# Optimization experiments

Hardware: AMD Instinct MI355X
Metric: run time of the kernel (lower is better)

The kernel has to match this reference:

```python
import jax, jax.numpy as jnp
import numpy as np

B, T, D, NPER, E = 32, 256, 1024, 64, 65536
N = B * NPER  # total nodes
LN_EPS = 1e-5


def setup_inputs() -> dict:
    key = jax.random.key(0)
    ks = jax.random.split(key, 12)
    sc = 0.02  # init scale for weights
    inp = {
        "x": jax.random.normal(ks[0], (B, T, D), jnp.float32),
        "batch": jnp.repeat(jnp.arange(B, dtype=jnp.int32), NPER),
        "edge_index": jax.random.randint(ks[1], (2, E), 0, N, dtype=jnp.int32),
        "edge_distance_vec": jax.random.normal(ks[2], (E, 3), jnp.float32),
        "edge_distance": jax.random.uniform(ks[3], (E,), jnp.float32) + 0.5,
        "natoms": NPER,
        # energy head params: LayerNorm -> Linear(D,D) -> GELU -> Linear(D,1)
        "ln_g": jnp.ones((D,), jnp.float32),
        "ln_b": jnp.zeros((D,), jnp.float32),
        "We1": jax.random.normal(ks[4], (D, D), jnp.float32) * sc,
        "be1": jnp.zeros((D,), jnp.float32),
        "We2": jax.random.normal(ks[5], (D, 1), jnp.float32) * sc,
        "be2": jnp.zeros((1,), jnp.float32),
        # forces head params: Linear(2D,D) -> GELU -> Linear(D,1)
        "Wf1": jax.random.normal(ks[6], (2 * D, D), jnp.float32) * sc,
        "bf1": jnp.zeros((D,), jnp.float32),
        "Wf2": jax.random.normal(ks[7], (D, 1), jnp.float32) * sc,
        "bf2": jnp.zeros((1,), jnp.float32),
    }
    return inp


def reference(x, batch, edge_index, edge_distance_vec, edge_distance, natoms,
              ln_g, ln_b, We1, be1, We2, be2, Wf1, bf1, Wf2, bf2):
    # ---- energy head on CLS token ----
    cls = x[:, 0]  # [B, D]
    mu = jnp.mean(cls, axis=-1, keepdims=True)
    var = jnp.mean(jnp.square(cls - mu), axis=-1, keepdims=True)
    h = (cls - mu) / jnp.sqrt(var + LN_EPS) * ln_g + ln_b
    h = jax.nn.gelu(h @ We1 + be1, approximate=False)
    energy = h @ We2 + be2  # [B, 1]

    # ---- forces head: gather node pairs -> MLP -> scale -> scatter-sum ----
    # padded_node_mask selects tokens 1..natoms per graph; boolean indexing
    # flattens row-major, identical to this slice+reshape.
    nodes = x[:, 1:1 + natoms].reshape(-1, x.shape[-1])  # [N, D]
    ei0, ei1 = edge_index[0], edge_index[1]
    edge_inputs = jnp.concatenate([nodes[ei0], nodes[ei1]], axis=1)  # [E, 2D]
    fm = jax.nn.gelu(edge_inputs @ Wf1 + bf1, approximate=False) @ Wf2 + bf2  # [E, 1]
    force_pairs = fm * edge_distance_vec / edge_distance[:, None]  # [E, 3]
    forces = jax.ops.segment_sum(force_pairs, ei0, num_segments=batch.shape[0])  # [N, 3]
    return energy, forces
```

## Files before the change

### kernel.cpp

```cpp
#include <hip/hip_runtime.h>
#include <hip/hip_fp16.h>
#include <math.h>

#define BB 32
#define TT 256
#define DD 1024
#define NNODES 2048
#define EE 65536
#define LN_EPS 1e-5f

typedef _Float16 halfx8 __attribute__((ext_vector_type(8)));
typedef __attribute__((ext_vector_type(4))) float floatx4;

__device__ __forceinline__ float gelu_fast(float x) {
    float x2 = x * x;
    float z = x * fmaf(0.10294456f, x2, 2.30211786f);
    float e = __builtin_amdgcn_exp2f(z);
    float r = __builtin_amdgcn_rcpf(1.0f + e);
    return fmaf(-x, r, x);
}

__device__ __forceinline__ __half2 gelu_h2(__half2 x) {
    const __half2 k = __float2half2_rn(-2.4554669f);
    const __half2 one = __float2half2_rn(1.0f);
    __half2 e = h2exp2(__hmul2(x, k));
    return __hmul2(x, h2rcp(__hadd2(e, one)));
}

__device__ __forceinline__ float dot2f(__half2 a, __half2 b, float c) {
#if __has_builtin(__builtin_amdgcn_fdot2)
    typedef _Float16 v2h __attribute__((ext_vector_type(2)));
    return __builtin_amdgcn_fdot2(*(v2h*)&a, *(v2h*)&b, c, false);
#else
    float2 af = __half22float2(a), bf = __half22float2(b);
    return fmaf(af.x, bf.x, fmaf(af.y, bf.y, c));
#endif
}

__device__ __forceinline__ unsigned short f32_to_h16(float f) {
    return __half_as_ushort(__float2half_rn(f));
}

__device__ __forceinline__ void load_lds16(const void* g, void* l) {
    __builtin_amdgcn_global_load_lds(
        (const __attribute__((address_space(1))) void*)g,
        (__attribute__((address_space(3))) void*)l, 16, 0, 0);
}

__global__ __launch_bounds__(256) void k1_zero_ln_prep_kernel(
    const float* __restrict__ x, const float* __restrict__ g,
    const float* __restrict__ bta, const float* __restrict__ Wf1,
    float* __restrict__ hnorm, float* __restrict__ out,
    unsigned short* __restrict__ nodesH, unsigned short* __restrict__ Wf1T) {
    __shared__ float smem[32 * 33];
    int t = threadIdx.x;
    int b = blockIdx.x;
    if (b < BB) {
        int zi = b * 256 + t;
        if (zi < BB + NNODES * 3) out[zi] = 0.0f;
        float* red = smem;
        const float* row = x + (size_t)b * TT * DD;
        float v[4];
        float s = 0.0f;
        #pragma unroll
        for (int j = 0; j < 4; ++j) { v[j] = row[t + j * 256]; s += v[j]; }
        red[t] = s; __syncthreads();
        for (int off = 128; off > 0; off >>= 1) {
            if (t < off) red[t] += red[t + off];
            __syncthreads();
        }
        float mu = red[0] * (1.0f / DD);
        __syncthreads();
        float sq = 0.0f;
        #pragma unroll
        for (int j = 0; j < 4; ++j) { float d = v[j] - mu; sq += d * d; }
        red[t] = sq; __syncthreads();
        for (int off = 128; off > 0; off >>= 1) {
            if (t < off) red[t] += red[t + off];
            __syncthreads();
        }
        float rstd = rsqrtf(red[0] * (1.0f / DD) + LN_EPS);
        #pragma unroll
        for (int j = 0; j < 4; ++j) {
            int d = t + j * 256;
            hnorm[b * DD + d] = (v[j] - mu) * rstd * g[d] + bta[d];
        }
        return;
    }
    int pb = b - BB;
    if (pb < 2048) {
        int idx4 = (pb * 256 + t) * 4;
        int i = idx4 >> 10;
        int k = idx4 & 1023;
        const float* src = x + ((size_t)(i >> 6) * TT + 1 + (i & 63)) * DD + k;
        float4 v = *(const float4*)src;
        ushort4 o;
        o.x = f32_to_h16(v.x); o.y = f32_to_h16(v.y);
        o.z = f32_to_h16(v.z); o.w = f32_to_h16(v.w);
        *(ushort4*)&nodesH[idx4] = o;
    } else {
        int q = pb - 2048;
        float (*tile)[33] = (float(*)[33])smem;
        int tx = t & 31;
        int ty = t >> 5;
        int n0 = (q & 31) * 32;
        int kg0 = (q >> 5) * 32;
        #pragma unroll
        for (int j = 0; j < 4; ++j) {
            int r = ty * 4 + j;
            tile[r][tx] = Wf1[(size_t)(kg0 + r) * DD + n0 + tx];
        }
        __syncthreads();
        int half = kg0 >> 10;
        int kk0 = kg0 & 1023;
        unsigned short* o = Wf1T + (size_t)half * DD * DD;
        #pragma unroll
        for (int j = 0; j < 4; ++j) {
            int rn = ty * 4 + j;
            o[(size_t)(n0 + rn) * DD + kk0 + tx] = f32_to_h16(tile[tx][rn]);
        }
    }
}

__global__ __launch_bounds__(512) void k2_gemm_kernel(
    const unsigned short* __restrict__ nodesH,
    const unsigned short* __restrict__ Wf1T, const float* __restrict__ bf1,
    unsigned short* __restrict__ P, const float* __restrict__ hnorm,
    const float* __restrict__ We1, float* __restrict__ He) {
    __shared__ unsigned short smem[2 * 128 * 64];
    int t = threadIdx.x;
    int b = blockIdx.x;
    if (b < 256) {
        unsigned short* As = smem;
        unsigned short* Bs = smem + 128 * 64;
        int w = t >> 6;
        int lane = t & 63;
        int quad = lane >> 4;
        int l16 = lane & 15;
        int wn = (w & 3) * 32;
        int wi = (w >> 2) * 64;
        int n0 = (b & 7) * 128;
        int i0 = ((b >> 3) & 15) * 128;
        int half = b >> 7;

        const unsigned short* Ag = Wf1T + (size_t)half * DD * DD;
        const unsigned short* Bg = nodesH;

        int sr = lane >> 3;
        int sc = (lane & 7) ^ sr;
        size_t aoff[2], boff[2];
        #pragma unroll
        for (int j = 0; j < 2; ++j) {
            int row = w * 16 + j * 8;
            aoff[j] = (size_t)(n0 + row + sr) * DD + sc * 8;
            boff[j] = (size_t)(i0 + row + sr) * DD + sc * 8;
        }

        floatx4 acc[2][4];
        #pragma unroll
        for (int a = 0; a < 2; ++a)
            #pragma unroll
            for (int c = 0; c < 4; ++c) {
                acc[a][c][0] = 0.f; acc[a][c][1] = 0.f;
                acc[a][c][2] = 0.f; acc[a][c][3] = 0.f;
            }

        for (int k0 = 0; k0 < DD; k0 += 64) {
            #pragma unroll
            for (int j = 0; j < 2; ++j) {
                int row = w * 16 + j * 8;
                load_lds16(Ag + aoff[j] + k0, (void*)(As + row * 64));
                load_lds16(Bg + boff[j] + k0, (void*)(Bs + row * 64));
            }
            __syncthreads();
            #pragma unroll
            for (int s = 0; s < 2; ++s) {
                halfx8 af[2], bfr[4];
                #pragma unroll
                for (int f = 0; f < 2; ++f) {
                    int rn = wn + f * 16 + l16;
                    af[f] = *(const halfx8*)&As[rn * 64 + ((((s << 2) | quad) ^ (rn & 7)) << 3)];
                }
                #pragma unroll
                for (int f = 0; f < 4; ++f) {
                    int ri = wi + f * 16 + l16;
                    bfr[f] = *(const halfx8*)&Bs[ri * 64 + ((((s << 2) | quad) ^ (ri & 7)) << 3)];
                }
                #pragma unroll
                for (int fa = 0; fa < 2; ++fa)
                    #pragma unroll
                    for (int fb = 0; fb < 4; ++fb)
                        acc[fa][fb] = __builtin_amdgcn_mfma_f32_16x16x32_f16(
                            af[fa], bfr[fb], acc[fa][fb], 0, 0, 0);
            }
            __syncthreads();
        }

        unsigned short* Pout = P + (size_t)half * NNODES * DD;
        #pragma unroll
        for (int fa = 0; fa < 2; ++fa) {
            int n = n0 + wn + fa * 16 + quad * 4;
            float4 badd = make_float4(0.f, 0.f, 0.f, 0.f);
            if (half == 0) badd = *(const float4*)(bf1 + n);
            #pragma unroll
            for (int fb = 0; fb < 4; ++fb) {
                int i = i0 + wi + fb * 16 + l16;
                floatx4 v = acc[fa][fb];
                ushort4 o;
                o.x = f32_to_h16(v[0] + badd.x);
                o.y = f32_to_h16(v[1] + badd.y);
                o.z = f32_to_h16(v[2] + badd.z);
                o.w = f32_to_h16(v[3] + badd.w);
                *(ushort4*)&Pout[(size_t)i * DD + n] = o;
            }
        }
        return;
    }
    {
        int q = b - 256;
        float* hs = (float*)smem;
        int col = (q & 1) * 512 + t;
        int k0 = ((q >> 1) & 15) * 64;
        int r0 = (q >> 5) * 16;
        for (int idx = t; idx < 64 * 16; idx += 512) {
            int r = idx & 15, k = idx >> 4;
            hs[idx] = hnorm[(size_t)(r0 + r) * DD + k0 + k];
        }
        __syncthreads();
        float acc[16];
        #pragma unroll
        for (int r = 0; r < 16; ++r) acc[r] = 0.0f;
        #pragma unroll 4
        for (int k = 0; k < 64; ++k) {
            float wv = We1[(size_t)(k0 + k) * DD + col];
            const float* hrow = hs + k * 16;
            #pragma unroll
            for (int j = 0; j < 4; ++j) {
                float4 h4 = *(const float4*)(hrow + j * 4);
                acc[j * 4 + 0] = fmaf(h4.x, wv, acc[j * 4 + 0]);
                acc[j * 4 + 1] = fmaf(h4.y, wv, acc[j * 4 + 1]);
                acc[j * 4 + 2] = fmaf(h4.z, wv, acc[j * 4 + 2]);
                acc[j * 4 + 3] = fmaf(h4.w, wv, acc[j * 4 + 3]);
            }
        }
        float* o = He + (size_t)((q >> 1) & 15) * 32 * DD;
        #pragma unroll
        for (int r = 0; r < 16; ++r) o[(size_t)(r0 + r) * DD + col] = acc[r];
    }
}

__global__ __launch_bounds__(256) void k3_edge_energy2_kernel(
    const unsigned short* __restrict__ P, const int* __restrict__ edge_index,
    const float* __restrict__ evec, const float* __restrict__ edist,
    const float* __restrict__ Wf2, const float* __restrict__ bf2,
    const float* __restrict__ He, const float* __restrict__ be1,
    const float* __restrict__ We2, const float* __restrict__ be2,
    float* __restrict__ out) {
    __shared__ float red[256];
    int t = threadIdx.x;
    int b = blockIdx.x;
    if (b < 4096) {
        float* forces = out + BB;
        int lane = t & 63;
        int wv = b * 4 + (t >> 6);
        int dbase = lane * 8;
        __half2 wh[8];
        #pragma unroll
        for (int s = 0; s < 2; ++s) {
            float4 a = *(const float4*)(Wf2 + s * 512 + dbase);
            float4 c = *(const float4*)(Wf2 + s * 512 + dbase + 4);
            wh[s * 4 + 0] = __floats2half2_rn(a.x, a.y);
            wh[s * 4 + 1] = __floats2half2_rn(a.z, a.w);
            wh[s * 4 + 2] = __floats2half2_rn(c.x, c.y);
            wh[s * 4 + 3] = __floats2half2_rn(c.z, c.w);
        }
        float bias2 = bf2[0];
        const unsigned short* P1 = P + (size_t)NNODES * DD;

        int i0v[4], i1v[4];
        #pragma unroll
        for (int j = 0; j < 4; ++j) {
            int e = wv + j * 16384;
            i0v[j] = __builtin_amdgcn_readfirstlane(edge_index[e]);
            i1v[j] = __builtin_amdgcn_readfirstlane(edge_index[EE + e]);
        }

        float4 buf[2][4];
        #pragma unroll
        for (int s = 0; s < 2; ++s) {
            buf[0][0 + s] = *(const float4*)(P  + (size_t)i0v[0] * DD + dbase + s * 512);
            buf[0][2 + s] = *(const float4*)(P1 + (size_t)i1v[0] * DD + dbase + s * 512);
        }
        float accs[2];
        #pragma unroll
        for (int j = 0; j < 4; ++j) {
            if (j < 3) {
                float4* nb = buf[(j + 1) & 1];
                #pragma unroll
                for (int s = 0; s < 2; ++s) {
                    nb[0 + s] = *(const float4*)(P  + (size_t)i0v[j + 1] * DD + dbase + s * 512);
                    nb[2 + s] = *(const float4*)(P1 + (size_t)i1v[j + 1] * DD + dbase + s * 512);
                }
            }
            const float4* cb = buf[j & 1];
            float acc = 0.0f;
            #pragma unroll
            for (int s = 0; s < 2; ++s) {
                const __half2* h0 = (const __half2*)&cb[s];
                const __half2* h1 = (const __half2*)&cb[2 + s];
                #pragma unroll
                for (int jj = 0; jj < 4; ++jj) {
                    __half2 hv = __hadd2(h0[jj], h1[jj]);
                    acc = dot2f(gelu_h2(hv), wh[s * 4 + jj], acc);
                }
            }
            accs[j & 1] = acc;
            if (j & 1) {
                float a0 = accs[0], a1 = accs[1];
                a0 += __shfl_xor(a0, 32, 64);
                a1 += __shfl_xor(a1, 32, 64);
                float r = (lane < 32) ? a0 : a1;
                #pragma unroll
                for (int off = 16; off > 0; off >>= 1) r += __shfl_xor(r, off, 64);
                float fm = r + bias2;
                int l5 = lane & 31;
                if (l5 < 3) {
                    int je = (lane < 32) ? (j - 1) : j;
                    int e = wv + je * 16384;
                    int i0 = (lane < 32) ? i0v[j - 1] : i0v[j];
                    float sc = fm / edist[e];
                    atomicAdd(&forces[i0 * 3 + l5], sc * evec[e * 3 + l5]);
                }
            }
        }
        return;
    }
    {
        int bb = b - 4096;
        float p = 0.0f;
        #pragma unroll
        for (int j = 0; j < 4; ++j) {
            int c = t * 4 + j;
            float s = 0.0f;
            #pragma unroll
            for (int ks = 0; ks < 16; ++ks)
                s += He[(size_t)ks * 32 * DD + bb * DD + c];
            s += be1[c];
            p += gelu_fast(s) * We2[c];
        }
        red[t] = p; __syncthreads();
        for (int off = 128; off > 0; off >>= 1) {
            if (t < off) red[t] += red[t + off];
            __syncthreads();
        }
        if (t == 0) out[bb] = red[0] + be2[0];
    }
}

extern "C" void kernel_launch(void* const* d_in, const int* in_sizes, int n_in,
                              void* d_out, int out_size, void* d_ws, size_t ws_size,
                              hipStream_t stream) {
    const float* x    = (const float*)d_in[0];
    const int* edge_index = (const int*)d_in[2];
    const float* evec = (const float*)d_in[3];
    const float* edist = (const float*)d_in[4];
    const float* ln_g = (const float*)d_in[6];
    const float* ln_b = (const float*)d_in[7];
    const float* We1  = (const float*)d_in[8];
    const float* be1  = (const float*)d_in[9];
    const float* We2  = (const float*)d_in[10];
    const float* be2  = (const float*)d_in[11];
    const float* Wf1  = (const float*)d_in[12];
    const float* bf1  = (const float*)d_in[13];
    const float* Wf2  = (const float*)d_in[14];
    const float* bf2  = (const float*)d_in[15];

    float* out = (float*)d_out;

    char* wsb = (char*)d_ws;
    unsigned short* P      = (unsigned short*)(wsb);
    float* hnorm           = (float*)(wsb + (8u << 20));
    float* He              = (float*)(wsb + (8u << 20) + (128u << 10));
    unsigned short* nodesH = (unsigned short*)(wsb + (11u << 20));
    unsigned short* Wf1T   = (unsigned short*)(wsb + (16u << 20));

    k1_zero_ln_prep_kernel<<<4128, 256, 0, stream>>>(x, ln_g, ln_b, Wf1, hnorm,
                                                     out, nodesH, Wf1T);
    k2_gemm_kernel<<<320, 512, 0, stream>>>(nodesH, Wf1T, bf1, P, hnorm, We1, He);
    k3_edge_energy2_kernel<<<4128, 256, 0, stream>>>(P, edge_index, evec, edist,
                                                     Wf2, bf2, He, be1, We2, be2,
                                                     out);
}
```

Baseline: 153.0 us.

## Sort edges by source node via counting sort and reduce forces per node

Result: slower. 181.2 us (+18.4%).

```diff
diff --git a/kernel.cpp b/kernel.cpp
--- a/kernel.cpp
+++ b/kernel.cpp
@@ -50,9 +50,12 @@
 __global__ __launch_bounds__(256) void k1_zero_ln_prep_kernel(
     const float* __restrict__ x, const float* __restrict__ g,
     const float* __restrict__ bta, const float* __restrict__ Wf1,
+    const int* __restrict__ edge_index,
     float* __restrict__ hnorm, float* __restrict__ out,
-    unsigned short* __restrict__ nodesH, unsigned short* __restrict__ Wf1T) {
+    unsigned short* __restrict__ nodesH, unsigned short* __restrict__ Wf1T,
+    int* __restrict__ hist_part) {
     __shared__ float smem[32 * 33];
+    __shared__ int hsh[2048];
     int t = threadIdx.x;
     int b = blockIdx.x;
     if (b < BB) {
@@ -98,7 +101,7 @@
         o.x = f32_to_h16(v.x); o.y = f32_to_h16(v.y);
         o.z = f32_to_h16(v.z); o.w = f32_to_h16(v.w);
         *(ushort4*)&nodesH[idx4] = o;
-    } else {
+    } else if (pb < 4096) {
         int q = pb - 2048;
         float (*tile)[33] = (float(*)[33])smem;
         int tx = t & 31;
@@ -119,6 +122,16 @@
             int rn = ty * 4 + j;
             o[(size_t)(n0 + rn) * DD + kk0 + tx] = f32_to_h16(tile[tx][rn]);
         }
+    } else {
+        int be = pb - 4096;
+        for (int i = t; i < 2048; i += 256) hsh[i] = 0;
+        __syncthreads();
+        int ebase = be * 8192 + t;
+        #pragma unroll 4
+        for (int i = 0; i < 32; ++i)
+            atomicAdd(&hsh[edge_index[ebase + i * 256]], 1);
+        __syncthreads();
+        for (int i = t; i < 2048; i += 256) hist_part[be * 2048 + i] = hsh[i];
     }
 }
 
@@ -126,7 +139,9 @@
     const unsigned short* __restrict__ nodesH,
     const unsigned short* __restrict__ Wf1T, const float* __restrict__ bf1,
     unsigned short* __restrict__ P, const float* __restrict__ hnorm,
-    const float* __restrict__ We1, float* __restrict__ He) {
+    const float* __restrict__ We1, float* __restrict__ He,
+    const int* __restrict__ hist_part, int* __restrict__ offs,
+    int* __restrict__ cnt, int* __restrict__ cursors) {
     __shared__ unsigned short smem[2 * 128 * 64];
     int t = threadIdx.x;
     int b = blockIdx.x;
@@ -216,6 +231,37 @@
         }
         return;
     }
+    if (b == 320) {
+        int* sh = (int*)smem;
+        int sums[4];
+        int g0 = t * 4;
+        int tot = 0;
+        #pragma unroll
+        for (int i = 0; i < 4; ++i) {
+            int s = 0;
+            #pragma unroll
+            for (int p = 0; p < 8; ++p) s += hist_part[p * 2048 + g0 + i];
+            sums[i] = tot;
+            tot += s;
+        }
+        sh[t] = tot; __syncthreads();
+        for (int off = 1; off < 512; off <<= 1) {
+            int v = (t >= off) ? sh[t - off] : 0;
+            __syncthreads();
+            sh[t] += v;
+            __syncthreads();
+        }
+        int basex = sh[t] - tot;
+        #pragma unroll
+        for (int i = 0; i < 4; ++i) {
+            int gbin = g0 + i;
+            int o = basex + sums[i];
+            offs[gbin] = o;
+            cursors[gbin] = o;
+            cnt[gbin] = ((i < 3) ? sums[i + 1] : tot) - sums[i];
+        }
+        return;
+    }
     {
         int q = b - 256;
         float* hs = (float*)smem;
@@ -249,20 +295,38 @@
     }
 }
 
+__global__ __launch_bounds__(256) void k2b_scatter_kernel(
+    const int* __restrict__ edge_index, int* __restrict__ cursors,
+    int* __restrict__ perm) {
+    int tid = blockIdx.x * 256 + threadIdx.x;
+    for (int e = tid; e < EE; e += 32 * 256) {
+        int i0 = edge_index[e];
+        int pos = atomicAdd(&cursors[i0], 1);
+        perm[pos] = e;
+    }
+}
+
 __global__ __launch_bounds__(256) void k3_edge_energy2_kernel(
     const unsigned short* __restrict__ P, const int* __restrict__ edge_index,
     const float* __restrict__ evec, const float* __restrict__ edist,
     const float* __restrict__ Wf2, const float* __restrict__ bf2,
     const float* __restrict__ He, const float* __restrict__ be1,
     const float* __restrict__ We2, const float* __restrict__ be2,
+    const int* __restrict__ offs, const int* __restrict__ cnt,
+    const int* __restrict__ perm,
     float* __restrict__ out) {
     __shared__ float red[256];
+    __shared__ float fred[2][3];
     int t = threadIdx.x;
     int b = blockIdx.x;
-    if (b < 4096) {
+    if (b < 1024) {
         float* forces = out + BB;
         int lane = t & 63;
-        int wv = b * 4 + (t >> 6);
+        int w = t >> 6;
+        int g = b * 2 + (w >> 1);
+        int half = w & 1;
+        if (t < 6) fred[t / 3][t % 3] = 0.0f;
+        __syncthreads();
         int dbase = lane * 8;
         __half2 wh[8];
         #pragma unroll
@@ -275,68 +339,75 @@
             wh[s * 4 + 3] = __floats2half2_rn(c.z, c.w);
         }
         float bias2 = bf2[0];
-        const unsigned short* P1 = P + (size_t)NNODES * DD;
-
-        int i0v[4], i1v[4];
-        #pragma unroll
-        for (int j = 0; j < 4; ++j) {
-            int e = wv + j * 16384;
-            i0v[j] = __builtin_amdgcn_readfirstlane(edge_index[e]);
-            i1v[j] = __builtin_amdgcn_readfirstlane(edge_index[EE + e]);
-        }
-
-        float4 buf[2][4];
-        #pragma unroll
-        for (int s = 0; s < 2; ++s) {
-            buf[0][0 + s] = *(const float4*)(P  + (size_t)i0v[0] * DD + dbase + s * 512);
-            buf[0][2 + s] = *(const float4*)(P1 + (size_t)i1v[0] * DD + dbase + s * 512);
-        }
-        float accs[2];
-        #pragma unroll
-        for (int j = 0; j < 4; ++j) {
-            if (j < 3) {
-                float4* nb = buf[(j + 1) & 1];
+        const unsigned short* P1g = P + (size_t)NNODES * DD;
+        int base = offs[g];
+        int cntg = cnt[g];
+        int cw = (cntg - half + 1) >> 1;
+        float4 p0a = *(const float4*)(P + (size_t)g * DD + dbase);
+        float4 p0b = *(const float4*)(P + (size_t)g * DD + dbase + 512);
+        float facc = 0.0f;
+        if (cw > 0) {
+            int e0 = perm[base + half];
+            int i10 = edge_index[EE + e0];
+            float4 c0 = *(const float4*)(P1g + (size_t)i10 * DD + dbase);
+            float4 c1 = *(const float4*)(P1g + (size_t)i10 * DD + dbase + 512);
+            float evl = (lane < 3) ? evec[e0 * 3 + lane] : 0.0f;
+            float dist = edist[e0];
+            int eA = 0, i1A = 0;
+            if (cw > 1) {
+                eA = perm[base + half + 2];
+                i1A = edge_index[EE + eA];
+            }
+            for (int j = 0; j < cw; ++j) {
+                bool more = (j + 1 < cw);
+                float4 n0, n1;
+                float evl2 = 0.0f, dist2 = 1.0f;
+                if (more) {
+                    n0 = *(const float4*)(P1g + (size_t)i1A * DD + dbase);
+                    n1 = *(const float4*)(P1g + (size_t)i1A * DD + dbase + 512);
+                    evl2 = (lane < 3) ? evec[eA * 3 + lane] : 0.0f;
+                    dist2 = edist[eA];
+                }
+                int eB = 0, i1B = 0;
+                if (j + 2 < cw) {
+                    eB = perm[base + half + 2 * (j + 2)];
+                    i1B = edge_index[EE + eB];
+                }
+                float acc = 0.0f;
+                {
+                    const __half2* h0 = (const __half2*)&p0a;
+                    const __half2* h1 = (const __half2*)&c0;
+                    #pragma unroll
+                    for (int jj = 0; jj < 4; ++jj) {
+                        __half2 hv = __hadd2(h0[jj], h1[jj]);
+                        acc = dot2f(gelu_h2(hv), wh[jj], acc);
+                    }
+                }
+                {
+                    const __half2* h0 = (const __half2*)&p0b;
+                    const __half2* h1 = (const __half2*)&c1;
+                    #pragma unroll
+                    for (int jj = 0; jj < 4; ++jj) {
+                        __half2 hv = __hadd2(h0[jj], h1[jj]);
+                        acc = dot2f(gelu_h2(hv), wh[4 + jj], acc);
+                    }
+                }
                 #pragma unroll
-                for (int s = 0; s < 2; ++s) {
-                    nb[0 + s] = *(const float4*)(P  + (size_t)i0v[j + 1] * DD + dbase + s * 512);
-                    nb[2 + s] = *(const float4*)(P1 + (size_t)i1v[j + 1] * DD + dbase + s * 512);
-                }
-            }
-            const float4* cb = buf[j & 1];
-            float acc = 0.0f;
-            #pragma unroll
-            for (int s = 0; s < 2; ++s) {
-                const __half2* h0 = (const __half2*)&cb[s];
-                const __half2* h1 = (const __half2*)&cb[2 + s];
-                #pragma unroll
-                for (int jj = 0; jj < 4; ++jj) {
-                    __half2 hv = __hadd2(h0[jj], h1[jj]);
-                    acc = dot2f(gelu_h2(hv), wh[s * 4 + jj], acc);
-                }
-            }
-            accs[j & 1] = acc;
-            if (j & 1) {
-                float a0 = accs[0], a1 = accs[1];
-                a0 += __shfl_xor(a0, 32, 64);
-                a1 += __shfl_xor(a1, 32, 64);
-                float r = (lane < 32) ? a0 : a1;
-                #pragma unroll
-                for (int off = 16; off > 0; off >>= 1) r += __shfl_xor(r, off, 64);
-                float fm = r + bias2;
-                int l5 = lane & 31;
-                if (l5 < 3) {
-                    int je = (lane < 32) ? (j - 1) : j;
-                    int e = wv + je * 16384;
-                    int i0 = (lane < 32) ? i0v[j - 1] : i0v[j];
-                    float sc = fm / edist[e];
-                    atomicAdd(&forces[i0 * 3 + l5], sc * evec[e * 3 + l5]);
-                }
-            }
-        }
+                for (int off = 32; off > 0; off >>= 1)
+                    acc += __shfl_xor(acc, off, 64);
+                float fm = acc + bias2;
+                facc += (fm / dist) * evl;
+                if (more) { c0 = n0; c1 = n1; evl = evl2; dist = dist2; }
+                if (j + 2 < cw) { eA = eB; i1A = i1B; }
+            }
+        }
+        if (lane < 3) atomicAdd(&fred[w >> 1][lane], facc);
+        __syncthreads();
+        if (t < 6) forces[b * 6 + t] = fred[t / 3][t % 3];
         return;
     }
     {
-        int bb = b - 4096;
+        int bb = b - 1024;
         float p = 0.0f;
         #pragma unroll
         for (int j = 0; j < 4; ++j) {
@@ -383,11 +454,19 @@
     float* He              = (float*)(wsb + (8u << 20) + (128u << 10));
     unsigned short* nodesH = (unsigned short*)(wsb + (11u << 20));
     unsigned short* Wf1T   = (unsigned short*)(wsb + (16u << 20));
-
-    k1_zero_ln_prep_kernel<<<4128, 256, 0, stream>>>(x, ln_g, ln_b, Wf1, hnorm,
-                                                     out, nodesH, Wf1T);
-    k2_gemm_kernel<<<320, 512, 0, stream>>>(nodesH, Wf1T, bf1, P, hnorm, We1, He);
-    k3_edge_energy2_kernel<<<4128, 256, 0, stream>>>(P, edge_index, evec, edist,
+    int* hist_part         = (int*)(wsb + (20u << 20));
+    int* offs              = hist_part + 8 * 2048;
+    int* cnt               = offs + 2048;
+    int* cursors           = cnt + 2048;
+    int* perm              = cursors + 2048;
+
+    k1_zero_ln_prep_kernel<<<4136, 256, 0, stream>>>(x, ln_g, ln_b, Wf1,
+                                                     edge_index, hnorm, out,
+                                                     nodesH, Wf1T, hist_part);
+    k2_gemm_kernel<<<321, 512, 0, stream>>>(nodesH, Wf1T, bf1, P, hnorm, We1,
+                                            He, hist_part, offs, cnt, cursors);
+    k2b_scatter_kernel<<<32, 256, 0, stream>>>(edge_index, cursors, perm);
+    k3_edge_energy2_kernel<<<1056, 256, 0, stream>>>(P, edge_index, evec, edist,
                                                      Wf2, bf2, He, be1, We2, be2,
-                                                     out);
-}
+                                                     offs, cnt, perm, out);
+}
```

## Sort edges by source node via counting sort before edge MLP

Applied to the files above, without the earlier changes.

After: 172.9 us. 1.13x slower.

```diff
diff --git a/kernel.cpp b/kernel.cpp
--- a/kernel.cpp
+++ b/kernel.cpp
@@ -50,9 +50,12 @@
 __global__ __launch_bounds__(256) void k1_zero_ln_prep_kernel(
     const float* __restrict__ x, const float* __restrict__ g,
     const float* __restrict__ bta, const float* __restrict__ Wf1,
+    const int* __restrict__ edge_index,
     float* __restrict__ hnorm, float* __restrict__ out,
-    unsigned short* __restrict__ nodesH, unsigned short* __restrict__ Wf1T) {
+    unsigned short* __restrict__ nodesH, unsigned short* __restrict__ Wf1T,
+    int* __restrict__ hist_part) {
     __shared__ float smem[32 * 33];
+    __shared__ int hsh[2048];
     int t = threadIdx.x;
     int b = blockIdx.x;
     if (b < BB) {
@@ -98,7 +101,7 @@
         o.x = f32_to_h16(v.x); o.y = f32_to_h16(v.y);
         o.z = f32_to_h16(v.z); o.w = f32_to_h16(v.w);
         *(ushort4*)&nodesH[idx4] = o;
-    } else {
+    } else if (pb < 4096) {
         int q = pb - 2048;
         float (*tile)[33] = (float(*)[33])smem;
         int tx = t & 31;
@@ -119,6 +122,16 @@
             int rn = ty * 4 + j;
             o[(size_t)(n0 + rn) * DD + kk0 + tx] = f32_to_h16(tile[tx][rn]);
         }
+    } else {
+        int be = pb - 4096;
+        for (int i = t; i < 2048; i += 256) hsh[i] = 0;
+        __syncthreads();
+        int ebase = be * 8192 + t;
+        #pragma unroll 4
+        for (int i = 0; i < 32; ++i)
+            atomicAdd(&hsh[edge_index[ebase + i * 256]], 1);
+        __syncthreads();
+        for (int i = t; i < 2048; i += 256) hist_part[be * 2048 + i] = hsh[i];
     }
 }
 
@@ -126,7 +139,9 @@
     const unsigned short* __restrict__ nodesH,
     const unsigned short* __restrict__ Wf1T, const float* __restrict__ bf1,
     unsigned short* __restrict__ P, const float* __restrict__ hnorm,
-    const float* __restrict__ We1, float* __restrict__ He) {
+    const float* __restrict__ We1, float* __restrict__ He,
+    const int* __restrict__ hist_part, int* __restrict__ offs,
+    int* __restrict__ cnt, int* __restrict__ cursors) {
     __shared__ unsigned short smem[2 * 128 * 64];
     int t = threadIdx.x;
     int b = blockIdx.x;
@@ -216,6 +231,37 @@
         }
         return;
     }
+    if (b == 320) {
+        int* sh = (int*)smem;
+        int sums[4];
+        int g0 = t * 4;
+        int tot = 0;
+        #pragma unroll
+        for (int i = 0; i < 4; ++i) {
+            int s = 0;
+            #pragma unroll
+            for (int p = 0; p < 8; ++p) s += hist_part[p * 2048 + g0 + i];
+            sums[i] = tot;
+            tot += s;
+        }
+        sh[t] = tot; __syncthreads();
+        for (int off = 1; off < 512; off <<= 1) {
+            int v = (t >= off) ? sh[t - off] : 0;
+            __syncthreads();
+            sh[t] += v;
+            __syncthreads();
+        }
+        int basex = sh[t] - tot;
+        #pragma unroll
+        for (int i = 0; i < 4; ++i) {
+            int gbin = g0 + i;
+            int o = basex + sums[i];
+            offs[gbin] = o;
+            cursors[gbin] = o;
+            cnt[gbin] = ((i < 3) ? sums[i + 1] : tot) - sums[i];
+        }
+        return;
+    }
     {
         int q = b - 256;
         float* hs = (float*)smem;
@@ -249,12 +295,24 @@
     }
 }
 
+__global__ __launch_bounds__(256) void k2b_scatter_kernel(
+    const int* __restrict__ edge_index, int* __restrict__ cursors,
+    int* __restrict__ perm) {
+    int tid = blockIdx.x * 256 + threadIdx.x;
+    for (int e = tid; e < EE; e += 32 * 256) {
+        int i0 = edge_index[e];
+        int pos = atomicAdd(&cursors[i0], 1);
+        perm[pos] = e;
+    }
+}
+
 __global__ __launch_bounds__(256) void k3_edge_energy2_kernel(
     const unsigned short* __restrict__ P, const int* __restrict__ edge_index,
     const float* __restrict__ evec, const float* __restrict__ edist,
     const float* __restrict__ Wf2, const float* __restrict__ bf2,
     const float* __restrict__ He, const float* __restrict__ be1,
     const float* __restrict__ We2, const float* __restrict__ be2,
+    const int* __restrict__ perm,
     float* __restrict__ out) {
     __shared__ float red[256];
     int t = threadIdx.x;
@@ -277,10 +335,11 @@
         float bias2 = bf2[0];
         const unsigned short* P1 = P + (size_t)NNODES * DD;
 
-        int i0v[4], i1v[4];
-        #pragma unroll
-        for (int j = 0; j < 4; ++j) {
-            int e = wv + j * 16384;
+        int ev[4], i0v[4], i1v[4];
+        #pragma unroll
+        for (int j = 0; j < 4; ++j) {
+            int e = __builtin_amdgcn_readfirstlane(perm[wv * 4 + j]);
+            ev[j] = e;
             i0v[j] = __builtin_amdgcn_readfirstlane(edge_index[e]);
             i1v[j] = __builtin_amdgcn_readfirstlane(edge_index[EE + e]);
         }
@@ -326,8 +385,8 @@
                 int l5 = lane & 31;
                 if (l5 < 3) {
                     int je = (lane < 32) ? (j - 1) : j;
-                    int e = wv + je * 16384;
-                    int i0 = (lane < 32) ? i0v[j - 1] : i0v[j];
+                    int e = ev[je];
+                    int i0 = i0v[je];
                     float sc = fm / edist[e];
                     atomicAdd(&forces[i0 * 3 + l5], sc * evec[e * 3 + l5]);
                 }
@@ -383,11 +442,19 @@
     float* He              = (float*)(wsb + (8u << 20) + (128u << 10));
     unsigned short* nodesH = (unsigned short*)(wsb + (11u << 20));
     unsigned short* Wf1T   = (unsigned short*)(wsb + (16u << 20));
-
-    k1_zero_ln_prep_kernel<<<4128, 256, 0, stream>>>(x, ln_g, ln_b, Wf1, hnorm,
-                                                     out, nodesH, Wf1T);
-    k2_gemm_kernel<<<320, 512, 0, stream>>>(nodesH, Wf1T, bf1, P, hnorm, We1, He);
+    int* hist_part         = (int*)(wsb + (20u << 20));
+    int* offs              = hist_part + 8 * 2048;
+    int* cnt               = offs + 2048;
+    int* cursors           = cnt + 2048;
+    int* perm              = cursors + 2048;
+
+    k1_zero_ln_prep_kernel<<<4136, 256, 0, stream>>>(x, ln_g, ln_b, Wf1,
+                                                     edge_index, hnorm, out,
+                                                     nodesH, Wf1T, hist_part);
+    k2_gemm_kernel<<<321, 512, 0, stream>>>(nodesH, Wf1T, bf1, P, hnorm, We1,
+                                            He, hist_part, offs, cnt, cursors);
+    k2b_scatter_kernel<<<32, 256, 0, stream>>>(edge_index, cursors, perm);
     k3_edge_energy2_kernel<<<4128, 256, 0, stream>>>(P, edge_index, evec, edist,
                                                      Wf2, bf2, He, be1, We2, be2,
-                                                     out);
-}
+                                                     perm, out);
+}
```
